# Performance work log

Hardware: AMD Instinct MI355X
Metric: run time of the kernel (lower is better)

## Reference

```python
import jax, jax.numpy as jnp
import numpy as np
from jax import lax

THRESHOLD = 1.0  # threshold_potential from __init__
STRIDE = (1, 1)
PADDING = 'SAME'


def setup_inputs() -> dict:
    key = jax.random.key(0)
    k1, k2, k3 = jax.random.split(key, 3)
    input_to_layer = jax.random.normal(k1, (1, 512, 512, 16), dtype=jnp.float32)
    weights = jax.random.normal(k2, (3, 3, 16, 64), dtype=jnp.float32)
    old_potentials = jax.random.normal(k3, (1, 512, 512, 64), dtype=jnp.float32)
    return {
        'input_to_layer': input_to_layer,
        'weights': weights,
        'old_potentials': old_potentials,
    }


def reference(input_to_layer, weights, old_potentials):
    # conv2d NHWC x HWIO -> NHWC, SAME padding, stride 1 (as tf.nn.conv2d)
    out_conv = lax.conv_general_dilated(
        input_to_layer, weights,
        window_strides=STRIDE, padding=PADDING,
        dimension_numbers=('NHWC', 'HWIO', 'NHWC'))
    # accumulate membrane potential, fused threshold -> spike + reset
    new_potentials = out_conv + old_potentials
    spiked = new_potentials >= THRESHOLD
    curr_spikes = spiked.astype(new_potentials.dtype)
    new_potentials = jnp.where(spiked, 0.0, new_potentials)
    # original returns spikes; new_potentials is the updated state
    return curr_spikes, new_potentials
```

## Files before the change

kernel.cpp:

```cpp
#include <hip/hip_runtime.h>


#define H 512
#define W 512
#define CI 16
#define CO 64
#define PW 514
#define PAD_PX (PW * PW)
#define KS 152
#define W_OFF_U16 0
#define IN_OFF_U16 32768

typedef float v4f __attribute__((ext_vector_type(4)));
typedef float f32x4 __attribute__((ext_vector_type(4)));
typedef short short8 __attribute__((ext_vector_type(8)));
typedef unsigned int uint4v __attribute__((ext_vector_type(4)));

__device__ __forceinline__ unsigned int pack2bf(float f0, float f1) {
    unsigned u0 = __builtin_bit_cast(unsigned, f0);
    unsigned u1 = __builtin_bit_cast(unsigned, f1);
    u0 = (u0 + 0x7FFFu + ((u0 >> 16) & 1u)) >> 16;
    u1 = (u1 + 0x7FFFu + ((u1 >> 16) & 1u)) >> 16;
    return u0 | (u1 << 16);
}

__global__ void snn_setup(const float* __restrict__ in,
                          const float* __restrict__ w,
                          unsigned short* __restrict__ ws)
{
    const int tid = threadIdx.x;
    if (blockIdx.x == gridDim.x - 1) {
        unsigned int* wsu = (unsigned int*)(ws + W_OFF_U16);
        const int n  = tid & 63;
        const int kq = tid >> 6;
        #pragma unroll
        for (int kk = 0; kk < 18; ++kk) {
            const int k = kq * 36 + kk * 2;
            const float f0 = w[k * CO + n];
            const float f1 = w[(k + 1) * CO + n];
            wsu[(n * KS + k) >> 1] = pack2bf(f0, f1);
        }
        if (kq == 3) {
            #pragma unroll
            for (int i = 0; i < 4; ++i)
                wsu[((n * KS + 144) >> 1) + i] = 0u;
        }
        return;
    }
    const int p = blockIdx.x * 256 + tid;
    if (p >= PAD_PX) return;
    const int py = p / PW, px = p - py * PW;
    uint4v pk0 = (uint4v)0u, pk1 = (uint4v)0u;
    if (py >= 1 && py <= H && px >= 1 && px <= W) {
        const v4f* q = (const v4f*)(in + ((py - 1) * W + (px - 1)) * CI);
        v4f a = q[0], b = q[1], c = q[2], d = q[3];
        pk0 = (uint4v){pack2bf(a.x, a.y), pack2bf(a.z, a.w),
                       pack2bf(b.x, b.y), pack2bf(b.z, b.w)};
        pk1 = (uint4v){pack2bf(c.x, c.y), pack2bf(c.z, c.w),
                       pack2bf(d.x, d.y), pack2bf(d.z, d.w)};
    }
    uint4v* dst = (uint4v*)(ws + IN_OFF_U16 + p * CI);
    dst[0] = pk0;
    dst[1] = pk1;
}

__global__ __launch_bounds__(256, 3)
void snn_conv_mfma(const unsigned short* __restrict__ ws,
                   const float* __restrict__ oldp,
                   float* __restrict__ out_spk,
                   float* __restrict__ out_pot)
{
    const unsigned short* pin = ws + IN_OFF_U16;
    const unsigned short* wsb = ws + W_OFF_U16;

    const int tid  = threadIdx.x;
    const int bx   = blockIdx.x & 31;
    const int by   = blockIdx.x >> 5;
    const int lane = tid & 63;
    const int wv   = tid >> 6;
    const int r    = lane & 15;
    const int quad = lane >> 4;
    const int half = quad & 1;
    const int tsel = quad >> 1;

    const int gy = by * 4 + wv;
    const int gx = bx * 16 + r;

    const int eb = (gy * W + gx) * CO + quad * 4;
    f32x4 oldv[4];
    #pragma unroll
    for (int nt = 0; nt < 4; ++nt)
        oldv[nt] = *(const f32x4*)(oldp + eb + nt * 16);

    short8 af[5];
    #pragma unroll
    for (int ks5 = 0; ks5 < 5; ++ks5) {
        const int t = (ks5 == 4) ? 8 : (2 * ks5 + tsel);
        const int dy = t / 3, dx = t % 3;
        af[ks5] = *(const short8*)&pin[((gy + dy) * PW + (gx + dx)) * CI + half * 8];
    }
    {
        const short8 zero8 = {0, 0, 0, 0, 0, 0, 0, 0};
        if (quad >= 2) af[4] = zero8;
    }

    f32x4 acc[4] = {};
    short8 bf_a[4], bf_b[4];

    #pragma unroll
    for (int nt = 0; nt < 4; ++nt)
        bf_a[nt] = *(const short8*)&wsb[(nt * 16 + r) * KS + quad * 8];

    #pragma unroll
    for (int ks5 = 0; ks5 < 5; ++ks5) {
        short8* cur = (ks5 & 1) ? bf_b : bf_a;
        short8* nxt = (ks5 & 1) ? bf_a : bf_b;
        if (ks5 < 4) {
            const int koff = (ks5 == 3) ? (128 + half * 8)
                                        : ((ks5 + 1) * 32 + quad * 8);
            #pragma unroll
            for (int nt = 0; nt < 4; ++nt)
                nxt[nt] = *(const short8*)&wsb[(nt * 16 + r) * KS + koff];
        }
        #pragma unroll
        for (int nt = 0; nt < 4; ++nt)
            acc[nt] = __builtin_amdgcn_mfma_f32_16x16x32_bf16(
                cur[nt], af[ks5], acc[nt], 0, 0, 0);
    }

    #pragma unroll
    for (int nt = 0; nt < 4; ++nt) {
        const int idx = eb + nt * 16;
        f32x4 np = acc[nt] + oldv[nt];
        f32x4 spk, pot;
        #pragma unroll
        for (int j = 0; j < 4; ++j) {
            const bool s = np[j] >= 1.0f;
            spk[j] = s ? 1.0f : 0.0f;
            pot[j] = s ? 0.0f : np[j];
        }
        *(f32x4*)(out_spk + idx) = spk;
        *(f32x4*)(out_pot + idx) = pot;
    }
}

extern "C" void kernel_launch(void* const* d_in, const int* in_sizes, int n_in,
                              void* d_out, int out_size, void* d_ws, size_t ws_size,
                              hipStream_t stream) {
    const float* in   = (const float*)d_in[0];
    const float* w    = (const float*)d_in[1];
    const float* oldp = (const float*)d_in[2];
    float* out_spk = (float*)d_out;
    float* out_pot = out_spk + (size_t)H * W * CO;
    unsigned short* ws = (unsigned short*)d_ws;

    const int setup_grid = (PAD_PX + 255) / 256 + 1;
    snn_setup<<<setup_grid, 256, 0, stream>>>(in, w, ws);

    const int grid = (W / 16) * (H / 4);
    snn_conv_mfma<<<grid, 256, 0, stream>>>(ws, oldp, out_spk, out_pot);
}
```

Before: 222.3 us.

## Persist weights in registers and software-pipeline eight row tiles per block

The conv kernel now has each block loop over eight row tiles instead of one. The block loads the full bf16 weight fragment set into registers once, and the setup kernel pre-swizzles the weights into MFMA lane order so those loads are contiguous. Input fragments and old potentials are prefetched three tiles ahead so global loads overlap MFMA work and stores. The grid shrinks to 512 blocks and launch bounds drop to 2 blocks per SM to fit the larger register footprint, which risks lower occupancy and fewer blocks to balance across CUs.

```diff
diff --git a/kernel.cpp b/kernel.cpp
--- a/kernel.cpp
+++ b/kernel.cpp
@@ -7,9 +7,10 @@
 #define CO 64
 #define PW 514
 #define PAD_PX (PW * PW)
-#define KS 152
-#define W_OFF_U16 0
+#define W3_OFF_U16 0
 #define IN_OFF_U16 32768
+#define NTILES 8
+#define PF 3
 
 typedef float v4f __attribute__((ext_vector_type(4)));
 typedef float f32x4 __attribute__((ext_vector_type(4)));
@@ -30,20 +31,25 @@
 {
     const int tid = threadIdx.x;
     if (blockIdx.x == gridDim.x - 1) {
-        unsigned int* wsu = (unsigned int*)(ws + W_OFF_U16);
-        const int n  = tid & 63;
-        const int kq = tid >> 6;
+        uint4v* wf = (uint4v*)(ws + W3_OFF_U16);
         #pragma unroll
-        for (int kk = 0; kk < 18; ++kk) {
-            const int k = kq * 36 + kk * 2;
-            const float f0 = w[k * CO + n];
-            const float f1 = w[(k + 1) * CO + n];
-            wsu[(n * KS + k) >> 1] = pack2bf(f0, f1);
-        }
-        if (kq == 3) {
+        for (int i = 0; i < 5; ++i) {
+            const int f    = i * 256 + tid;
+            const int ks5  = f >> 8;
+            const int rem  = f & 255;
+            const int nt   = rem >> 6;
+            const int lane = rem & 63;
+            const int r    = lane & 15;
+            const int quad = lane >> 4;
+            const int k0   = (ks5 < 4) ? (ks5 * 32 + quad * 8)
+                                       : (128 + (quad & 1) * 8);
+            const int co   = nt * 16 + r;
+            uint4v v;
             #pragma unroll
-            for (int i = 0; i < 4; ++i)
-                wsu[((n * KS + 144) >> 1) + i] = 0u;
+            for (int m = 0; m < 4; ++m)
+                v[m] = pack2bf(w[(k0 + 2 * m) * CO + co],
+                               w[(k0 + 2 * m + 1) * CO + co]);
+            wf[f] = v;
         }
         return;
     }
@@ -64,18 +70,17 @@
     dst[1] = pk1;
 }
 
-__global__ __launch_bounds__(256, 3)
+__global__ __launch_bounds__(256, 2)
 void snn_conv_mfma(const unsigned short* __restrict__ ws,
                    const float* __restrict__ oldp,
                    float* __restrict__ out_spk,
                    float* __restrict__ out_pot)
 {
     const unsigned short* pin = ws + IN_OFF_U16;
-    const unsigned short* wsb = ws + W_OFF_U16;
 
     const int tid  = threadIdx.x;
     const int bx   = blockIdx.x & 31;
-    const int by   = blockIdx.x >> 5;
+    const int g    = blockIdx.x >> 5;
     const int lane = tid & 63;
     const int wv   = tid >> 6;
     const int r    = lane & 15;
@@ -83,64 +88,68 @@
     const int half = quad & 1;
     const int tsel = quad >> 1;
 
-    const int gy = by * 4 + wv;
-    const int gx = bx * 16 + r;
+    const int gx  = bx * 16 + r;
+    const int gyB = g * (4 * NTILES) + wv;
 
-    const int eb = (gy * W + gx) * CO + quad * 4;
-    f32x4 oldv[4];
+    short8 bf[5][4];
     #pragma unroll
-    for (int nt = 0; nt < 4; ++nt)
-        oldv[nt] = *(const f32x4*)(oldp + eb + nt * 16);
+    for (int ks5 = 0; ks5 < 5; ++ks5)
+        #pragma unroll
+        for (int nt = 0; nt < 4; ++nt)
+            bf[ks5][nt] = *(const short8*)&ws[(ks5 * 256 + nt * 64 + lane) * 8];
 
-    short8 af[5];
-    #pragma unroll
-    for (int ks5 = 0; ks5 < 5; ++ks5) {
-        const int t = (ks5 == 4) ? 8 : (2 * ks5 + tsel);
-        const int dy = t / 3, dx = t % 3;
-        af[ks5] = *(const short8*)&pin[((gy + dy) * PW + (gx + dx)) * CI + half * 8];
-    }
-    {
-        const short8 zero8 = {0, 0, 0, 0, 0, 0, 0, 0};
-        if (quad >= 2) af[4] = zero8;
-    }
+    short8 af[NTILES][5];
+    f32x4  oldv[NTILES][4];
 
-    f32x4 acc[4] = {};
-    short8 bf_a[4], bf_b[4];
+    auto issue = [&](int t) {
+        const int gy = gyB + t * 4;
+        const int eb = (gy * W + gx) * CO + quad * 4;
+        #pragma unroll
+        for (int nt = 0; nt < 4; ++nt)
+            oldv[t][nt] = *(const f32x4*)(oldp + eb + nt * 16);
+        #pragma unroll
+        for (int ks5 = 0; ks5 < 4; ++ks5) {
+            const int t8 = 2 * ks5 + tsel;
+            const int dy = t8 / 3, dx = t8 % 3;
+            af[t][ks5] = *(const short8*)
+                &pin[((gy + dy) * PW + (gx + dx)) * CI + half * 8];
+        }
+        const int p4 = (quad < 2) ? ((gy + 2) * PW + (gx + 2)) : gx;
+        af[t][4] = *(const short8*)&pin[p4 * CI + half * 8];
+    };
+
+    issue(0);
+    issue(1);
+    issue(2);
 
     #pragma unroll
-    for (int nt = 0; nt < 4; ++nt)
-        bf_a[nt] = *(const short8*)&wsb[(nt * 16 + r) * KS + quad * 8];
-
-    #pragma unroll
-    for (int ks5 = 0; ks5 < 5; ++ks5) {
-        short8* cur = (ks5 & 1) ? bf_b : bf_a;
-        short8* nxt = (ks5 & 1) ? bf_a : bf_b;
-        if (ks5 < 4) {
-            const int koff = (ks5 == 3) ? (128 + half * 8)
-                                        : ((ks5 + 1) * 32 + quad * 8);
+    for (int t = 0; t < NTILES; ++t) {
+        f32x4 acc[4] = {};
+        #pragma unroll
+        for (int ks5 = 0; ks5 < 5; ++ks5)
             #pragma unroll
             for (int nt = 0; nt < 4; ++nt)
-                nxt[nt] = *(const short8*)&wsb[(nt * 16 + r) * KS + koff];
+                acc[nt] = __builtin_amdgcn_mfma_f32_16x16x32_bf16(
+                    bf[ks5][nt], af[t][ks5], acc[nt], 0, 0, 0);
+
+        const int gy = gyB + t * 4;
+        const int eb = (gy * W + gx) * CO + quad * 4;
+        #pragma unroll
+        for (int nt = 0; nt < 4; ++nt) {
+            const int idx = eb + nt * 16;
+            f32x4 np = acc[nt] + oldv[t][nt];
+            f32x4 spk, pot;
+            #pragma unroll
+            for (int j = 0; j < 4; ++j) {
+                const bool s = np[j] >= 1.0f;
+                spk[j] = s ? 1.0f : 0.0f;
+                pot[j] = s ? 0.0f : np[j];
+            }
+            *(f32x4*)(out_spk + idx) = spk;
+            *(f32x4*)(out_pot + idx) = pot;
         }
-        #pragma unroll
-        for (int nt = 0; nt < 4; ++nt)
-            acc[nt] = __builtin_amdgcn_mfma_f32_16x16x32_bf16(
-                cur[nt], af[ks5], acc[nt], 0, 0, 0);
-    }
 
-    #pragma unroll
-    for (int nt = 0; nt < 4; ++nt) {
-        const int idx = eb + nt * 16;
-        f32x4 np = acc[nt] + oldv[nt];
-        f32x4 spk, pot;
-        #pragma unroll
-        for (int j = 0; j < 4; ++j) {
-            const bool s = np[j] >= 1.0f;
-            spk[j] = s ? 1.0f : 0.0f;
-            pot[j] = s ? 0.0f : np[j];
-        }
-        *(f32x4*)(out_spk + idx) = spk;
-        *(f32x4*)(out_pot + idx) = pot;
+        if (t + PF < NTILES) issue(t + PF);
     }
 }
 
@@ -157,6 +166,6 @@
     const int setup_grid = (PAD_PX + 255) / 256 + 1;
     snn_setup<<<setup_grid, 256, 0, stream>>>(in, w, ws);
 
-    const int grid = (W / 16) * (H / 4);
+    const int grid = 32 * 16;
     snn_conv_mfma<<<grid, 256, 0, stream>>>(ws, oldp, out_spk, out_pot);
 }
```

After: 231.9 us. 1.04x slower.
